# Kernel optimization log

Hardware: AMD Instinct MI355X
Metric: run time of the kernel (lower is better)

Reference implementation:

```python
import jax, jax.numpy as jnp
import numpy as np
from jax import lax

K = 3          # kernel_size
STRIDE = 2
BN_EPS = 1e-5
CLAMP_MIN = 1e-4


def setup_inputs() -> dict:
    key = jax.random.key(0)
    k1, k2 = jax.random.split(key)
    x = jax.random.normal(k1, (16, 64, 112, 112), dtype=jnp.float32)
    # kaiming-normal fan_out init: std = sqrt(2 / (out_ch * kh * kw))
    std = np.sqrt(2.0 / (9 * 3 * 3)).astype(np.float32)
    conv_w = jax.random.normal(k2, (9, 64, 3, 3), dtype=jnp.float32) * std
    gamma = jnp.ones((9,), dtype=jnp.float32)
    beta = jnp.zeros((9,), dtype=jnp.float32)
    return {"x": x, "conv_w": conv_w, "gamma": gamma, "beta": beta}


def reference(x, conv_w, gamma, beta):
    p = K // 2
    n, c, h, w = x.shape
    xp = jnp.pad(x, ((0, 0), (0, 0), (p, p), (p, p)), mode="reflect")  # [n,c,h+2p,w+2p]

    # sigma = BN(conv(pad(x))) with 3x3 conv, stride 1, no bias -> [n, k*k, h, w]
    sigma = lax.conv_general_dilated(
        xp, conv_w, window_strides=(1, 1), padding="VALID",
        dimension_numbers=("NCHW", "OIHW", "NCHW"))
    mean = jnp.mean(sigma, axis=(0, 2, 3), keepdims=True)
    var = jnp.var(sigma, axis=(0, 2, 3), keepdims=True)
    sigma = (sigma - mean) * lax.rsqrt(var + BN_EPS)
    sigma = sigma * gamma[None, :, None, None] + beta[None, :, None, None]
    sigma = jnp.clip(sigma, CLAMP_MIN)               # clamp(min=1e-4)
    sigma = sigma / jnp.sum(sigma, axis=1, keepdims=True)  # normalize over k*k taps

    # unfold pad(x) into k*k patches -> [n, c*k*k, h, w] (channel-major like torch unfold)
    patches = lax.conv_general_dilated_patches(
        xp, filter_shape=(K, K), window_strides=(1, 1), padding="VALID",
        dimension_numbers=("NCHW", "OIHW", "NCHW"))
    patches = patches.reshape(n, c, K * K, h, w)

    out = jnp.sum(patches * sigma[:, None], axis=2)  # [n, c, h, w]
    return out[:, :, ::STRIDE, ::STRIDE]
```

## Files before the change

### kernel.cpp

```cpp
#include <hip/hip_runtime.h>
#include <math.h>

namespace {

constexpr int Hh = 112, Ww = 112, Cc = 64, Nn = 16;
constexpr int OHh = 56, OWw = 56;
constexpr int HW = Hh * Ww;
constexpr int OP = OHh * OWw;
constexpr int NP = Nn * OP;
constexpr int NHW = Nn * HW;
constexpr float BN_EPS_F = 1e-5f;
constexpr float CLAMP_MIN_F = 1e-4f;
constexpr int NSTAT = 32;

typedef float f4 __attribute__((ext_vector_type(4)));
typedef f4 f4u __attribute__((aligned(4)));

struct WSet { f4 v[3]; };

__device__ __forceinline__ void load_set(WSet& s, const float* __restrict__ base,
                                         const int (&ro)[3], int wb) {
#pragma unroll
    for (int r = 0; r < 3; ++r)
        s.v[r] = *(const f4u*)(base + ro[r] + wb);
}

__device__ __forceinline__ void compute_set(const WSet& s, const float* __restrict__ wgt,
                                            int cg, bool ez, bool eh,
                                            float (&acc0)[9], float (&acc1)[9]) {
    float el[3], m0[3], m1[3], er[3];
#pragma unroll
    for (int r = 0; r < 3; ++r) {
        const f4 v = s.v[r];
        el[r] = (ez || eh) ? v.y : v.x;
        m0[r] = ez ? v.x : (eh ? v.z : v.y);
        m1[r] = ez ? v.y : (eh ? v.w : v.z);
        er[r] = (ez || eh) ? v.z : v.w;
    }
#pragma unroll
    for (int k = 0; k < 9; ++k) {
        const float* wk = wgt + ((size_t)k * Cc + cg) * 9;
#pragma unroll
        for (int r = 0; r < 3; ++r) {
            const float wa = wk[3 * r], wb = wk[3 * r + 1], wc = wk[3 * r + 2];
            acc0[k] = fmaf(wa, el[r], acc0[k]);
            acc0[k] = fmaf(wb, m0[r], acc0[k]);
            acc0[k] = fmaf(wc, m1[r], acc0[k]);
            acc1[k] = fmaf(wa, m0[r], acc1[k]);
            acc1[k] = fmaf(wb, m1[r], acc1[k]);
            acc1[k] = fmaf(wc, er[r], acc1[k]);
        }
    }
}

template <int NSPLIT>
__global__ __launch_bounds__(256) void conv_2deep_kernel(
    const float* __restrict__ x, const float* __restrict__ wgt,
    float* __restrict__ P )
{
    constexpr int CHS = Cc / NSPLIT;
    constexpr int NBLK = NSPLIT * 392;

    const int tid = threadIdx.x;
    const int b = blockIdx.x;
    const int swz = (b & 7) * (NBLK / 8) + (b >> 3);
    const int part = swz / 392;
    const int bid = swz - part * 392;

    const int s = bid * 256 + tid;
    const int pos0 = 2 * s;
    const int n = pos0 / HW;
    const int hw = pos0 - n * HW;
    const int h = hw / Ww;
    const int w0 = hw - h * Ww;

    const int hm = (h == 0) ? 1 : h - 1;
    const int hp = (h == Hh - 1) ? (Hh - 2) : (h + 1);
    const bool ez = (w0 == 0), eh = (w0 == Ww - 2);
    const int wb = ez ? 0 : (eh ? (Ww - 4) : (w0 - 1));

    const int ro[3] = { hm * Ww, h * Ww, hp * Ww };

    const float* xb = x + ((size_t)n * Cc + part * CHS) * HW;

    float acc0[9], acc1[9];
#pragma unroll
    for (int k = 0; k < 9; ++k) { acc0[k] = 0.f; acc1[k] = 0.f; }

    WSet A, B, C;
    load_set(A, xb, ro, wb);
    load_set(B, xb + HW, ro, wb);

#define STEP(c, SC, SF)                                                          \
    if constexpr ((c) < CHS) {                                                   \
        if constexpr ((c) + 2 < CHS)                                             \
            load_set(SF, xb + (size_t)((c) + 2) * HW, ro, wb);                   \
        compute_set(SC, wgt, part * CHS + (c), ez, eh, acc0, acc1);              \
    }

    STEP(0,  A, C) STEP(1,  B, A) STEP(2,  C, B)
    STEP(3,  A, C) STEP(4,  B, A) STEP(5,  C, B)
    STEP(6,  A, C) STEP(7,  B, A) STEP(8,  C, B)
    STEP(9,  A, C) STEP(10, B, A) STEP(11, C, B)
    STEP(12, A, C) STEP(13, B, A) STEP(14, C, B)
    STEP(15, A, C) STEP(16, B, A) STEP(17, C, B)
    STEP(18, A, C) STEP(19, B, A) STEP(20, C, B)
    STEP(21, A, C) STEP(22, B, A) STEP(23, C, B)
    STEP(24, A, C) STEP(25, B, A) STEP(26, C, B)
    STEP(27, A, C) STEP(28, B, A) STEP(29, C, B)
    STEP(30, A, C) STEP(31, B, A)
#undef STEP

    float* Ph = P + (size_t)part * 9 * NHW;
#pragma unroll
    for (int k = 0; k < 9; ++k)
        *(float2*)(Ph + (size_t)k * NHW + pos0) = make_float2(acc0[k], acc1[k]);
}

template <int NSPLIT>
__global__ __launch_bounds__(256) void merge_stats_kernel(
    const float* __restrict__ P, double* __restrict__ stats,
    float* __restrict__ sig_even )
{
    __shared__ float rs[4], rq[4];
    const int tid = threadIdx.x;
    const int k = blockIdx.y;
    const int p0 = (blockIdx.x * 256 + tid) * 4;

    float4 v = *(const float4*)(P + (size_t)k * NHW + p0);
#pragma unroll
    for (int qq = 1; qq < NSPLIT; ++qq) {
        const float4 t = *(const float4*)(P + ((size_t)qq * 9 + k) * NHW + p0);
        v.x += t.x; v.y += t.y; v.z += t.z; v.w += t.w;
    }

    const int w = p0 % Ww;
    const int h = (p0 / Ww) % Hh;
    const int n = p0 / HW;
    if (!(h & 1)) {
        *(float2*)(sig_even + (size_t)k * NP + n * OP + (h >> 1) * OWw + (w >> 1)) =
            make_float2(v.x, v.z);
    }

    float s = v.x + v.y + v.z + v.w;
    float q = v.x * v.x + v.y * v.y + v.z * v.z + v.w * v.w;
#pragma unroll
    for (int off = 32; off > 0; off >>= 1) {
        s += __shfl_down(s, off, 64);
        q += __shfl_down(q, off, 64);
    }
    const int lane = tid & 63, wv = tid >> 6;
    if (lane == 0) { rs[wv] = s; rq[wv] = q; }
    __syncthreads();
    if (tid == 0) {
        double* st = stats + (size_t)(blockIdx.x & (NSTAT - 1)) * 18;
        atomicAdd(&st[k], (double)(rs[0] + rs[1] + rs[2] + rs[3]));
        atomicAdd(&st[9 + k], (double)(rq[0] + rq[1] + rq[2] + rq[3]));
    }
}

__global__ __launch_bounds__(256) void apply_kernel(
    const float* __restrict__ x, const float* __restrict__ sig_raw,
    const float* __restrict__ gamma, const float* __restrict__ beta,
    const double* __restrict__ stats, float* __restrict__ out)
{
    __shared__ float srow[9][OWw];
    __shared__ float mean_s[9], istd_s[9], gb[18];

    const int tid = threadIdx.x;
    const int f = blockIdx.x;
    const int swz = (f & 7) * 448 + (f >> 3);
    const int q = swz / 896;
    const int fs = swz - q * 896;
    const int n = fs / OHh;
    const int oh = fs % OHh;

    if (tid < 9) {
        double s = 0.0, qq = 0.0;
        for (int r = 0; r < NSTAT; ++r) { s += stats[r * 18 + tid]; qq += stats[r * 18 + 9 + tid]; }
        const double cnt = (double)Nn * HW;
        const double m = s / cnt;
        const double v = qq / cnt - m * m;
        mean_s[tid] = (float)m;
        istd_s[tid] = (float)(1.0 / sqrt(v + (double)BN_EPS_F));
        gb[tid] = gamma[tid];
        gb[9 + tid] = beta[tid];
    }
    __syncthreads();

    if (tid < OWw) {
        const int pp = n * OP + oh * OWw + tid;
        float s[9], ssum = 0.f;
#pragma unroll
        for (int k = 0; k < 9; ++k) {
            float v = fmaf((sig_raw[(size_t)k * NP + pp] - mean_s[k]) * istd_s[k], gb[k], gb[9 + k]);
            v = fmaxf(v, CLAMP_MIN_F);
            s[k] = v;
            ssum += v;
        }
        const float inv = 1.f / ssum;
#pragma unroll
        for (int k = 0; k < 9; ++k) srow[k][tid] = s[k] * inv;
    }
    __syncthreads();

    const int csub = tid >> 6;
    const int lane = tid & 63;
    if (lane >= OWw) return;
    const int ow = lane;

    const int r0 = (oh == 0) ? 1 : (2 * oh - 1);
    const int r1 = 2 * oh, r2 = 2 * oh + 1;
    const bool ez = (ow == 0), eh = (ow == OWw - 1);
    const int wb = ez ? 0 : (eh ? (Ww - 4) : (2 * ow - 1));
    const int rr[3] = { r0 * Ww + wb, r1 * Ww + wb, r2 * Ww + wb };

    float sg[9];
#pragma unroll
    for (int k = 0; k < 9; ++k) sg[k] = srow[k][ow];

#pragma unroll
    for (int cc = 0; cc < 4; ++cc) {
        const int c = q * 16 + cc * 4 + csub;
        const float* xc = x + ((size_t)(n * Cc + c)) * HW;
        float o = 0.f;
#pragma unroll
        for (int r = 0; r < 3; ++r) {
            const f4 v = *(const f4u*)(xc + rr[r]);
            const float a0 = (ez || eh) ? v.y : v.x;
            const float a1 = ez ? v.x : (eh ? v.z : v.y);
            const float a2 = ez ? v.y : (eh ? v.w : v.z);
            o = fmaf(sg[3 * r], a0, o);
            o = fmaf(sg[3 * r + 1], a1, o);
            o = fmaf(sg[3 * r + 2], a2, o);
        }
        out[((size_t)(n * Cc + c)) * OP + oh * OWw + ow] = o;
    }
}

}

extern "C" void kernel_launch(void* const* d_in, const int* in_sizes, int n_in,
                              void* d_out, int out_size, void* d_ws, size_t ws_size,
                              hipStream_t stream) {
    const float* x     = (const float*)d_in[0];
    const float* wgt   = (const float*)d_in[1];
    const float* gamma = (const float*)d_in[2];
    const float* beta  = (const float*)d_in[3];
    float* out = (float*)d_out;

    double* stats = (double*)d_ws;
    float* P = (float*)((char*)d_ws + 8192);

    const size_t sig_bytes = (size_t)9 * NP * 4;
    const size_t need4 = 8192 + (size_t)36 * NHW * 4 + sig_bytes;
    hipMemsetAsync(d_ws, 0, 8192, stream);

    if (ws_size >= need4) {
        float* sig_even = P + (size_t)36 * NHW;
        conv_2deep_kernel<4><<<1568, 256, 0, stream>>>(x, wgt, P);
        merge_stats_kernel<4><<<dim3(196, 9), 256, 0, stream>>>(P, stats, sig_even);
        apply_kernel<<<3584, 256, 0, stream>>>(x, sig_even, gamma, beta, stats, out);
    } else {
        float* sig_even = P + (size_t)18 * NHW;
        conv_2deep_kernel<2><<<784, 256, 0, stream>>>(x, wgt, P);
        merge_stats_kernel<2><<<dim3(196, 9), 256, 0, stream>>>(P, stats, sig_even);
        apply_kernel<<<3584, 256, 0, stream>>>(x, sig_even, gamma, beta, stats, out);
    }
}
```

Before: 72.27 us.

## Fuse channel-split conv reduction and BN stats into one kernel via LDS

Replaces the grid-level channel split, which wrote partial conv sums to global memory and then merged them in a separate kernel, with an in-block split. Each of the four waves handles 16 channels for the same 128 pixels, and the partials are reduced through shared memory. The same block then writes the even-position sigma values and accumulates the BN sum and sum of squares with atomics. This removes a large global partial buffer round-trip and one kernel launch, at the cost of extra syncthreads, LDS traffic, and only half the threads taking part in the final stats.

```diff
diff --git a/kernel.cpp b/kernel.cpp
--- a/kernel.cpp
+++ b/kernel.cpp
@@ -53,22 +53,21 @@
     }
 }
 
-template <int NSPLIT>
-__global__ __launch_bounds__(256) void conv_2deep_kernel(
+__global__ __launch_bounds__(256) void conv_stats_kernel(
     const float* __restrict__ x, const float* __restrict__ wgt,
-    float* __restrict__ P )
+    double* __restrict__ stats, float* __restrict__ sig_even )
 {
-    constexpr int CHS = Cc / NSPLIT;
-    constexpr int NBLK = NSPLIT * 392;
+    __shared__ float red[2][128][9];
+    __shared__ float rsum[2][9], rsq[2][9];
 
     const int tid = threadIdx.x;
+    const int lane = tid & 63;
+    const int wv = __builtin_amdgcn_readfirstlane(tid >> 6);
+
     const int b = blockIdx.x;
-    const int swz = (b & 7) * (NBLK / 8) + (b >> 3);
-    const int part = swz / 392;
-    const int bid = swz - part * 392;
-
-    const int s = bid * 256 + tid;
-    const int pos0 = 2 * s;
+    const int swz = (b & 7) * 196 + (b >> 3);
+
+    const int pos0 = swz * 128 + 2 * lane;
     const int n = pos0 / HW;
     const int hw = pos0 - n * HW;
     const int h = hw / Ww;
@@ -81,7 +80,8 @@
 
     const int ro[3] = { hm * Ww, h * Ww, hp * Ww };
 
-    const float* xb = x + ((size_t)n * Cc + part * CHS) * HW;
+    const float* xb = x + ((size_t)n * Cc + wv * 16) * HW;
+    const int cbase = wv * 16;
 
     float acc0[9], acc1[9];
 #pragma unroll
@@ -92,10 +92,10 @@
     load_set(B, xb + HW, ro, wb);
 
 #define STEP(c, SC, SF)                                                          \
-    if constexpr ((c) < CHS) {                                                   \
-        if constexpr ((c) + 2 < CHS)                                             \
+    {                                                                            \
+        if constexpr ((c) + 2 < 16)                                              \
             load_set(SF, xb + (size_t)((c) + 2) * HW, ro, wb);                   \
-        compute_set(SC, wgt, part * CHS + (c), ez, eh, acc0, acc1);              \
+        compute_set(SC, wgt, cbase + (c), ez, eh, acc0, acc1);                   \
     }
 
     STEP(0,  A, C) STEP(1,  B, A) STEP(2,  C, B)
@@ -103,59 +103,63 @@
     STEP(6,  A, C) STEP(7,  B, A) STEP(8,  C, B)
     STEP(9,  A, C) STEP(10, B, A) STEP(11, C, B)
     STEP(12, A, C) STEP(13, B, A) STEP(14, C, B)
-    STEP(15, A, C) STEP(16, B, A) STEP(17, C, B)
-    STEP(18, A, C) STEP(19, B, A) STEP(20, C, B)
-    STEP(21, A, C) STEP(22, B, A) STEP(23, C, B)
-    STEP(24, A, C) STEP(25, B, A) STEP(26, C, B)
-    STEP(27, A, C) STEP(28, B, A) STEP(29, C, B)
-    STEP(30, A, C) STEP(31, B, A)
+    STEP(15, A, C)
 #undef STEP
 
-    float* Ph = P + (size_t)part * 9 * NHW;
-#pragma unroll
-    for (int k = 0; k < 9; ++k)
-        *(float2*)(Ph + (size_t)k * NHW + pos0) = make_float2(acc0[k], acc1[k]);
-}
-
-template <int NSPLIT>
-__global__ __launch_bounds__(256) void merge_stats_kernel(
-    const float* __restrict__ P, double* __restrict__ stats,
-    float* __restrict__ sig_even )
-{
-    __shared__ float rs[4], rq[4];
-    const int tid = threadIdx.x;
-    const int k = blockIdx.y;
-    const int p0 = (blockIdx.x * 256 + tid) * 4;
-
-    float4 v = *(const float4*)(P + (size_t)k * NHW + p0);
-#pragma unroll
-    for (int qq = 1; qq < NSPLIT; ++qq) {
-        const float4 t = *(const float4*)(P + ((size_t)qq * 9 + k) * NHW + p0);
-        v.x += t.x; v.y += t.y; v.z += t.z; v.w += t.w;
-    }
-
-    const int w = p0 % Ww;
-    const int h = (p0 / Ww) % Hh;
-    const int n = p0 / HW;
-    if (!(h & 1)) {
-        *(float2*)(sig_even + (size_t)k * NP + n * OP + (h >> 1) * OWw + (w >> 1)) =
-            make_float2(v.x, v.z);
-    }
-
-    float s = v.x + v.y + v.z + v.w;
-    float q = v.x * v.x + v.y * v.y + v.z * v.z + v.w * v.w;
-#pragma unroll
-    for (int off = 32; off > 0; off >>= 1) {
-        s += __shfl_down(s, off, 64);
-        q += __shfl_down(q, off, 64);
-    }
-    const int lane = tid & 63, wv = tid >> 6;
-    if (lane == 0) { rs[wv] = s; rq[wv] = q; }
-    __syncthreads();
-    if (tid == 0) {
-        double* st = stats + (size_t)(blockIdx.x & (NSTAT - 1)) * 18;
-        atomicAdd(&st[k], (double)(rs[0] + rs[1] + rs[2] + rs[3]));
-        atomicAdd(&st[9 + k], (double)(rq[0] + rq[1] + rq[2] + rq[3]));
+    if (wv >= 2) {
+#pragma unroll
+        for (int k = 0; k < 9; ++k) {
+            red[wv - 2][2 * lane][k] = acc0[k];
+            red[wv - 2][2 * lane + 1][k] = acc1[k];
+        }
+    }
+    __syncthreads();
+    if (wv < 2) {
+#pragma unroll
+        for (int k = 0; k < 9; ++k) {
+            red[wv][2 * lane][k] += acc0[k];
+            red[wv][2 * lane + 1][k] += acc1[k];
+        }
+    }
+    __syncthreads();
+
+    float sig[9];
+    if (tid < 128) {
+#pragma unroll
+        for (int k = 0; k < 9; ++k) sig[k] = red[0][tid][k] + red[1][tid][k];
+
+        const int pos = swz * 128 + tid;
+        const int n2 = pos / HW;
+        const int hw2 = pos - n2 * HW;
+        const int h2 = hw2 / Ww;
+        const int w2 = hw2 - h2 * Ww;
+        if (!(h2 & 1) && !(w2 & 1)) {
+            float* sp = sig_even + (size_t)0 * NP + n2 * OP + (h2 >> 1) * OWw + (w2 >> 1);
+#pragma unroll
+            for (int k = 0; k < 9; ++k) sp[(size_t)k * NP] = sig[k];
+        }
+    } else {
+#pragma unroll
+        for (int k = 0; k < 9; ++k) sig[k] = 0.f;
+    }
+
+#pragma unroll
+    for (int k = 0; k < 9; ++k) {
+        float s = sig[k], q = sig[k] * sig[k];
+#pragma unroll
+        for (int off = 32; off > 0; off >>= 1) {
+            s += __shfl_down(s, off, 64);
+            q += __shfl_down(q, off, 64);
+        }
+        if (wv < 2 && lane == 0) { rsum[wv][k] = s; rsq[wv][k] = q; }
+    }
+    __syncthreads();
+    if (tid < 9) {
+        const float s = rsum[0][tid] + rsum[1][tid];
+        const float q = rsq[0][tid] + rsq[1][tid];
+        double* st = stats + (size_t)(swz & (NSTAT - 1)) * 18;
+        atomicAdd(&st[tid], (double)s);
+        atomicAdd(&st[9 + tid], (double)q);
     }
 }
 
@@ -250,21 +254,9 @@
     float* out = (float*)d_out;
 
     double* stats = (double*)d_ws;
-    float* P = (float*)((char*)d_ws + 8192);
-
-    const size_t sig_bytes = (size_t)9 * NP * 4;
-    const size_t need4 = 8192 + (size_t)36 * NHW * 4 + sig_bytes;
+    float* sig_even = (float*)((char*)d_ws + 8192);
+
     hipMemsetAsync(d_ws, 0, 8192, stream);
-
-    if (ws_size >= need4) {
-        float* sig_even = P + (size_t)36 * NHW;
-        conv_2deep_kernel<4><<<1568, 256, 0, stream>>>(x, wgt, P);
-        merge_stats_kernel<4><<<dim3(196, 9), 256, 0, stream>>>(P, stats, sig_even);
-        apply_kernel<<<3584, 256, 0, stream>>>(x, sig_even, gamma, beta, stats, out);
-    } else {
-        float* sig_even = P + (size_t)18 * NHW;
-        conv_2deep_kernel<2><<<784, 256, 0, stream>>>(x, wgt, P);
-        merge_stats_kernel<2><<<dim3(196, 9), 256, 0, stream>>>(P, stats, sig_even);
-        apply_kernel<<<3584, 256, 0, stream>>>(x, sig_even, gamma, beta, stats, out);
-    }
-}
+    conv_stats_kernel<<<1568, 256, 0, stream>>>(x, wgt, stats, sig_even);
+    apply_kernel<<<3584, 256, 0, stream>>>(x, sig_even, gamma, beta, stats, out);
+}
```

Measured after the change: 78.03 us. +8.0%, slower.
